# Performance work log

Hardware: AMD Instinct MI355X
Metric: run time of the kernel (lower is better)

## Reference

```python
import jax, jax.numpy as jnp
import numpy as np

B, H, W = 8, 512, 512          # batch, detector grid
M_PER_B = 32768
N = B * M_PER_B
C_IN, C_OUT, RED = 64, 128, 4
EPS = 1e-5


def setup_inputs() -> dict:
    key = jax.random.key(0)
    ks = jax.random.split(key, 8)
    # unique active-site indices per batch (permutation of flat grid cells)
    rng = np.random.default_rng(0)
    rows = []
    for b in range(B):
        flat = rng.permutation(H * W)[:M_PER_B]
        y, x = flat // W, flat % W
        rows.append(np.stack([np.full(M_PER_B, b), y, x], axis=1))
    indices = jnp.asarray(np.concatenate(rows, 0), dtype=jnp.int32)  # [N,3]

    feats = jax.random.normal(ks[0], (N, C_IN), jnp.float32)
    s1 = 1.0 / np.sqrt(9 * C_IN)
    s2 = 1.0 / np.sqrt(9 * C_OUT)
    return {
        "feats": feats,
        "indices": indices,
        "bn1_g": jnp.ones((C_IN,), jnp.float32),
        "bn1_b": jnp.zeros((C_IN,), jnp.float32),
        "w1": jax.random.normal(ks[1], (9, C_IN, C_OUT), jnp.float32) * s1,
        "bn2_g": jnp.ones((C_OUT,), jnp.float32),
        "bn2_b": jnp.zeros((C_OUT,), jnp.float32),
        "w2": jax.random.normal(ks[2], (9, C_OUT, C_OUT), jnp.float32) * s2,
        "fc1_w": jax.random.normal(ks[3], (C_OUT // RED, C_OUT), jnp.float32) / np.sqrt(C_OUT),
        "fc1_b": jnp.zeros((C_OUT // RED,), jnp.float32),
        "fc2_w": jax.random.normal(ks[4], (C_OUT, C_OUT // RED), jnp.float32) / np.sqrt(C_OUT // RED),
        "fc2_b": jnp.zeros((C_OUT,), jnp.float32),
        "w_skip": jax.random.normal(ks[5], (C_IN, C_OUT), jnp.float32) / np.sqrt(C_IN),
    }


def build_rulebook(indices):
    """Neighbor point-ids for each 3x3 offset. Returns ids [N,9], mask [N,9]."""
    n = indices.shape[0]
    b, y, x = indices[:, 0], indices[:, 1], indices[:, 2]
    grid = jnp.full((B, H, W), -1, jnp.int32).at[b, y, x].set(
        jnp.arange(n, dtype=jnp.int32))
    ids, masks = [], []
    for dy in (-1, 0, 1):
        for dx in (-1, 0, 1):
            ny, nx = y + dy, x + dx
            inb = (ny >= 0) & (ny < H) & (nx >= 0) & (nx < W)
            nid = grid[b, jnp.clip(ny, 0, H - 1), jnp.clip(nx, 0, W - 1)]
            m = inb & (nid >= 0)
            ids.append(jnp.where(m, nid, 0))
            masks.append(m)
    return jnp.stack(ids, 1), jnp.stack(masks, 1)


def subm_conv(f, nbr_ids, nbr_mask, w):
    """Submanifold 3x3 conv: gather-GEMM-scatter over active sites."""
    out = jnp.zeros((f.shape[0], w.shape[2]), f.dtype)
    for k in range(w.shape[0]):  # fixed 9 kernel offsets
        g = jnp.where(nbr_mask[:, k:k + 1], f[nbr_ids[:, k]], 0.0)
        out = out + g @ w[k]
    return out


def batchnorm(x, g, b):
    m = jnp.mean(x, 0)
    v = jnp.var(x, 0)  # biased, matches torch BN training normalization
    return (x - m) * jax.lax.rsqrt(v + EPS) * g + b


def reference(feats, indices, bn1_g, bn1_b, w1, bn2_g, bn2_b, w2,
              fc1_w, fc1_b, fc2_w, fc2_b, w_skip):
    nbr_ids, nbr_mask = build_rulebook(indices)  # shared indice_key rulebook
    bidx = indices[:, 0]

    out = jax.nn.relu(batchnorm(feats, bn1_g, bn1_b))
    out = subm_conv(out, nbr_ids, nbr_mask, w1)
    out = jax.nn.relu(batchnorm(out, bn2_g, bn2_b))
    out = subm_conv(out, nbr_ids, nbr_mask, w2)

    # SE: scatter-mean pool per event, FC-ReLU-FC-Sigmoid, per-site rescale
    pooled = jax.ops.segment_sum(out, bidx, num_segments=B)
    counts = jax.ops.segment_sum(jnp.ones((out.shape[0], 1), out.dtype), bidx,
                                 num_segments=B)
    pooled = pooled / jnp.clip(counts, 1.0, None)
    se = jax.nn.sigmoid(jax.nn.relu(pooled @ fc1_w.T + fc1_b) @ fc2_w.T + fc2_b)
    out = out * se[bidx]

    identity = feats @ w_skip  # 1x1 subm conv skip (in_ch != out_ch)
    return out + identity
```

## Files before the change

### kernel.cpp

```cpp
#include <hip/hip_runtime.h>
#include <math.h>

#define NPTS 262144
#define BB 8
#define HH 512
#define WW 512
#define EPSV 1e-5f

typedef short short8v __attribute__((ext_vector_type(8)));
typedef short short4v __attribute__((ext_vector_type(4)));
typedef float float4v __attribute__((ext_vector_type(4)));
typedef unsigned short ushort;
typedef ushort ushort8v __attribute__((ext_vector_type(8)));

static __device__ __forceinline__ ushort f2bf(float f) {
  union { float f; unsigned u; } v;
  v.f = f;
  unsigned r = v.u + 0x7fffu + ((v.u >> 16) & 1u);
  return (ushort)(r >> 16);
}

static __device__ __forceinline__ float bf2f(ushort h) {
  union { unsigned u; float f; } v;
  v.u = ((unsigned)h) << 16;
  return v.f;
}


__global__ __launch_bounds__(256) void k_scatter(const int* __restrict__ idx,
                                                 int* __restrict__ grid) {
  int i = blockIdx.x * 256 + threadIdx.x;
  int b = idx[i * 3 + 0], y = idx[i * 3 + 1], x = idx[i * 3 + 2];
  grid[(b * HH + y) * WW + x] = i;
}

__global__ __launch_bounds__(256) void k_rulebook(const int* __restrict__ idx,
                                                  const int* __restrict__ grid,
                                                  int* __restrict__ nbrT) {
  int i = blockIdx.x * 256 + threadIdx.x;
  int b = idx[i * 3 + 0], y = idx[i * 3 + 1], x = idx[i * 3 + 2];
  int t = 0;
  #pragma unroll
  for (int dy = -1; dy <= 1; ++dy) {
    #pragma unroll
    for (int dx = -1; dx <= 1; ++dx) {
      int ny = y + dy, nx = x + dx;
      int v = -1;
      if (ny >= 0 && ny < HH && nx >= 0 && nx < WW)
        v = grid[(b * HH + ny) * WW + nx];
      nbrT[(size_t)t * NPTS + i] = v;
      ++t;
    }
  }
}


__global__ __launch_bounds__(256) void k_stats64(const float* __restrict__ x,
                                                 float* __restrict__ sum,
                                                 float* __restrict__ ssum) {
  __shared__ float red_s[4][64];
  __shared__ float red_q[4][64];
  const int tid = threadIdx.x;
  const int lane = tid & 63;
  const int wave = tid >> 6;
  const int c4 = lane & 15;
  const int rq = lane >> 4;
  long long base = (long long)blockIdx.x * 256;
  float s0 = 0.f, s1 = 0.f, s2 = 0.f, s3 = 0.f;
  float q0 = 0.f, q1 = 0.f, q2 = 0.f, q3 = 0.f;
  for (int r = wave * 4 + rq; r < 256; r += 16) {
    float4 v = *(const float4*)(x + (base + r) * 64 + c4 * 4);
    s0 += v.x; s1 += v.y; s2 += v.z; s3 += v.w;
    q0 += v.x * v.x; q1 += v.y * v.y; q2 += v.z * v.z; q3 += v.w * v.w;
  }
  s0 += __shfl_xor(s0, 16, 64); s0 += __shfl_xor(s0, 32, 64);
  s1 += __shfl_xor(s1, 16, 64); s1 += __shfl_xor(s1, 32, 64);
  s2 += __shfl_xor(s2, 16, 64); s2 += __shfl_xor(s2, 32, 64);
  s3 += __shfl_xor(s3, 16, 64); s3 += __shfl_xor(s3, 32, 64);
  q0 += __shfl_xor(q0, 16, 64); q0 += __shfl_xor(q0, 32, 64);
  q1 += __shfl_xor(q1, 16, 64); q1 += __shfl_xor(q1, 32, 64);
  q2 += __shfl_xor(q2, 16, 64); q2 += __shfl_xor(q2, 32, 64);
  q3 += __shfl_xor(q3, 16, 64); q3 += __shfl_xor(q3, 32, 64);
  if (rq == 0) {
    red_s[wave][c4 * 4 + 0] = s0; red_s[wave][c4 * 4 + 1] = s1;
    red_s[wave][c4 * 4 + 2] = s2; red_s[wave][c4 * 4 + 3] = s3;
    red_q[wave][c4 * 4 + 0] = q0; red_q[wave][c4 * 4 + 1] = q1;
    red_q[wave][c4 * 4 + 2] = q2; red_q[wave][c4 * 4 + 3] = q3;
  }
  __syncthreads();
  if (tid < 64) {
    float ts = red_s[0][tid] + red_s[1][tid] + red_s[2][tid] + red_s[3][tid];
    float tq = red_q[0][tid] + red_q[1][tid] + red_q[2][tid] + red_q[3][tid];
    atomicAdd(&sum[tid], ts);
    atomicAdd(&ssum[tid], tq);
  }
}

template <int CI>
__global__ void k_finalize(const float* __restrict__ sum, const float* __restrict__ ssum,
                           const float* __restrict__ gam, const float* __restrict__ bet,
                           float* __restrict__ sc, float* __restrict__ sh) {
  int c = threadIdx.x;
  if (c < CI) {
    float m = sum[c] * (1.f / NPTS);
    float v = ssum[c] * (1.f / NPTS) - m * m;
    float s = gam[c] * rsqrtf(v + EPSV);
    sc[c] = s;
    sh[c] = bet[c] - m * s;
  }
}


__global__ __launch_bounds__(256) void k_norm1(const float* __restrict__ x,
                                               const float* __restrict__ sc,
                                               const float* __restrict__ sh,
                                               ushort* __restrict__ y) {
  long long i = ((long long)blockIdx.x * 256 + threadIdx.x) * 8;
  int c = (int)(i & 63);
  float4 a = *(const float4*)(x + i);
  float4 b = *(const float4*)(x + i + 4);
  float4 s0 = *(const float4*)(sc + c);
  float4 s1 = *(const float4*)(sc + c + 4);
  float4 h0 = *(const float4*)(sh + c);
  float4 h1 = *(const float4*)(sh + c + 4);
  ushort8v o;
  o[0] = f2bf(fmaxf(a.x * s0.x + h0.x, 0.f));
  o[1] = f2bf(fmaxf(a.y * s0.y + h0.y, 0.f));
  o[2] = f2bf(fmaxf(a.z * s0.z + h0.z, 0.f));
  o[3] = f2bf(fmaxf(a.w * s0.w + h0.w, 0.f));
  o[4] = f2bf(fmaxf(b.x * s1.x + h1.x, 0.f));
  o[5] = f2bf(fmaxf(b.y * s1.y + h1.y, 0.f));
  o[6] = f2bf(fmaxf(b.z * s1.z + h1.z, 0.f));
  o[7] = f2bf(fmaxf(b.w * s1.w + h1.w, 0.f));
  *(ushort8v*)(y + i) = o;
}

__global__ __launch_bounds__(256) void k_norm2(ushort* __restrict__ x,
                                               const float* __restrict__ sc,
                                               const float* __restrict__ sh) {
  long long i = ((long long)blockIdx.x * 256 + threadIdx.x) * 8;
  int c = (int)(i & 127);
  ushort8v v = *(const ushort8v*)(x + i);
  float4 s0 = *(const float4*)(sc + c);
  float4 s1 = *(const float4*)(sc + c + 4);
  float4 h0 = *(const float4*)(sh + c);
  float4 h1 = *(const float4*)(sh + c + 4);
  ushort8v o;
  o[0] = f2bf(fmaxf(bf2f(v[0]) * s0.x + h0.x, 0.f));
  o[1] = f2bf(fmaxf(bf2f(v[1]) * s0.y + h0.y, 0.f));
  o[2] = f2bf(fmaxf(bf2f(v[2]) * s0.z + h0.z, 0.f));
  o[3] = f2bf(fmaxf(bf2f(v[3]) * s0.w + h0.w, 0.f));
  o[4] = f2bf(fmaxf(bf2f(v[4]) * s1.x + h1.x, 0.f));
  o[5] = f2bf(fmaxf(bf2f(v[5]) * s1.y + h1.y, 0.f));
  o[6] = f2bf(fmaxf(bf2f(v[6]) * s1.z + h1.z, 0.f));
  o[7] = f2bf(fmaxf(bf2f(v[7]) * s1.w + h1.w, 0.f));
  *(ushort8v*)(x + i) = o;
}


__global__ __launch_bounds__(256) void k_wprep(const float* __restrict__ w,
                                               ushort* __restrict__ wt,
                                               int taps, int ci) {
  int i = blockIdx.x * 256 + threadIdx.x;
  int total = taps * ci * 128;
  if (i < total) {
    int t = i / (ci * 128);
    int rem = i - t * ci * 128;
    int c = rem >> 7;
    int o = rem & 127;
    wt[((size_t)t * 128 + o) * ci + c] = f2bf(w[i]);
  }
}


template <int CI, typename DstT, int EPI>
__global__ __launch_bounds__(256) void k_convp(const ushort* __restrict__ src,
                                               const int* __restrict__ nbrT,
                                               const ushort* __restrict__ wt,
                                               DstT* __restrict__ dst,
                                               float* __restrict__ e0,
                                               float* __restrict__ e1) {
  constexpr int CHUNKS = CI / 8;
  constexpr int RPI    = 64 / CHUNKS;
  constexpr int NSTG   = 32 / RPI;
  __shared__ ushort As[128 * CI];

  const int tid = threadIdx.x;
  int bidx = blockIdx.x;
  bidx = (bidx & 7) * ((NPTS / 128) / 8) + (bidx >> 3);
  const int base = bidx * 128;
  const int lane = tid & 63;
  const int wave = tid >> 6;
  const int wm = wave & 1, wn = wave >> 1;
  const int m_base = wm * 64, n_base = wn * 64;
  const int fm = lane & 15;
  const int fq = lane >> 4;

  const int s_rl = lane / CHUNKS;
  const int s_c  = lane % CHUNKS;
  const int srow0 = wave * 32 + s_rl;

  float4v acc[4][4];
  #pragma unroll
  for (int i = 0; i < 4; ++i)
    #pragma unroll
    for (int j = 0; j < 4; ++j) acc[i][j] = (float4v){0.f, 0.f, 0.f, 0.f};

  int nr[2][NSTG];
  uint4 g[NSTG];

  #pragma unroll
  for (int i = 0; i < NSTG; ++i)
    nr[0][i] = nbrT[base + srow0 + i * RPI];
  #pragma unroll
  for (int i = 0; i < NSTG; ++i)
    nr[1][i] = nbrT[(size_t)NPTS + base + srow0 + i * RPI];

  #pragma unroll
  for (int i = 0; i < NSTG; ++i) {
    int nid = nr[0][i];
    uint4 gv = {0u, 0u, 0u, 0u};
    if (nid >= 0) gv = *(const uint4*)(src + (size_t)nid * CI + s_c * 8);
    g[i] = gv;
  }
  #pragma unroll
  for (int i = 0; i < NSTG; ++i) {
    int row = srow0 + i * RPI;
    *(uint4*)(&As[row * CI + ((s_c ^ (row & 7)) << 3)]) = g[i];
  }
  __syncthreads();

  #pragma unroll
  for (int k = 0; k < 9; ++k) {
    if (k < 8) {
      #pragma unroll
      for (int i = 0; i < NSTG; ++i) {
        int nid = nr[(k + 1) & 1][i];
        uint4 gv = {0u, 0u, 0u, 0u};
        if (nid >= 0) gv = *(const uint4*)(src + (size_t)nid * CI + s_c * 8);
        g[i] = gv;
      }
    }
    if (k < 7) {
      #pragma unroll
      for (int i = 0; i < NSTG; ++i)
        nr[k & 1][i] = nbrT[(size_t)(k + 2) * NPTS + base + srow0 + i * RPI];
    }

    const ushort* wrow = wt + ((size_t)k * 128 + n_base + fm) * CI + fq * 8;
    #pragma unroll
    for (int kc = 0; kc < CI / 32; ++kc) {
      short8v af[4], bfr[4];
      #pragma unroll
      for (int mi = 0; mi < 4; ++mi) {
        int R = m_base + mi * 16 + fm;
        af[mi] = *(const short8v*)(&As[R * CI + (((kc * 4 + fq) ^ (fm & 7)) << 3)]);
      }
      #pragma unroll
      for (int ni = 0; ni < 4; ++ni)
        bfr[ni] = *(const short8v*)(wrow + ni * 16 * CI + kc * 32);
      #pragma unroll
      for (int mi = 0; mi < 4; ++mi)
        #pragma unroll
        for (int ni = 0; ni < 4; ++ni)
          acc[mi][ni] = __builtin_amdgcn_mfma_f32_16x16x32_bf16(af[mi], bfr[ni], acc[mi][ni], 0, 0, 0);
    }

    if (k < 8) {
      __syncthreads();
      #pragma unroll
      for (int i = 0; i < NSTG; ++i) {
        int row = srow0 + i * RPI;
        *(uint4*)(&As[row * CI + ((s_c ^ (row & 7)) << 3)]) = g[i];
      }
      __syncthreads();
    }
  }

  float es[4], ess[4];
  if constexpr (EPI) {
    #pragma unroll
    for (int ni = 0; ni < 4; ++ni) { es[ni] = 0.f; ess[ni] = 0.f; }
  }
  #pragma unroll
  for (int mi = 0; mi < 4; ++mi) {
    #pragma unroll
    for (int ni = 0; ni < 4; ++ni) {
      int pt = base + m_base + mi * 16 + fq * 4;
      int co = n_base + ni * 16 + fm;
      float4v c = acc[mi][ni];
      #pragma unroll
      for (int r = 0; r < 4; ++r) {
        if constexpr (sizeof(DstT) == 4) {
          ((float*)dst)[(size_t)(pt + r) * 128 + co] = c[r];
          if constexpr (EPI == 2) es[ni] += c[r];
        } else {
          ushort h = f2bf(c[r]);
          ((ushort*)dst)[(size_t)(pt + r) * 128 + co] = h;
          if constexpr (EPI == 1) {
            float v = bf2f(h);
            es[ni] += v;
            ess[ni] += v * v;
          }
        }
      }
    }
  }

  if constexpr (EPI) {
    #pragma unroll
    for (int ni = 0; ni < 4; ++ni) {
      float s = es[ni];
      s += __shfl_xor(s, 16, 64);
      s += __shfl_xor(s, 32, 64);
      float q = 0.f;
      if constexpr (EPI == 1) {
        q = ess[ni];
        q += __shfl_xor(q, 16, 64);
        q += __shfl_xor(q, 32, 64);
      }
      if (fq == 0) {
        int co = n_base + ni * 16 + fm;
        if constexpr (EPI == 1) {
          atomicAdd(&e0[co], s);
          atomicAdd(&e1[co], q);
        } else {
          int b = base >> 15;
          atomicAdd(&e0[b * 128 + co], s);
        }
      }
    }
  }
}


template <typename SrcT, typename DstT, int CI, int TAPS, bool ACT, int EPI>
__global__ __launch_bounds__(256) void k_conv(const SrcT* __restrict__ src,
                                              const float* __restrict__ scale,
                                              const float* __restrict__ shift,
                                              const int* __restrict__ nbrT,
                                              const ushort* __restrict__ wt,
                                              DstT* __restrict__ dst,
                                              float* __restrict__ e0,
                                              float* __restrict__ e1) {
  constexpr int SA = CI + 8;
  __shared__ ushort As[128 * SA];
  __shared__ ushort Bs[128 * SA];
  __shared__ float s_sc[CI], s_sh[CI];

  const int tid = threadIdx.x;
  const int base = blockIdx.x * 128;
  const int lane = tid & 63;
  const int wave = tid >> 6;
  const int wm = wave & 1, wn = wave >> 1;
  const int m_base = wm * 64, n_base = wn * 64;
  const int fm = lane & 15;
  const int fq = lane >> 4;

  if constexpr (ACT) {
    for (int c = tid; c < CI; c += 256) {
      s_sc[c] = scale[c];
      s_sh[c] = shift[c];
    }
  }
  __syncthreads();

  float4v acc[4][4];
  #pragma unroll
  for (int i = 0; i < 4; ++i)
    #pragma unroll
    for (int j = 0; j < 4; ++j) acc[i][j] = (float4v){0.f, 0.f, 0.f, 0.f};

  const int srow_i = tid >> 1;
  const int shalf = tid & 1;
  const int c0 = shalf * (CI / 2);

  for (int k = 0; k < TAPS; ++k) {
    if (k) __syncthreads();

    int nid;
    if constexpr (TAPS == 1) {
      nid = base + srow_i;
    } else {
      nid = nbrT[(size_t)k * NPTS + base + srow_i];
    }
    ushort* arow = &As[srow_i * SA + c0];
    if (nid >= 0) {
      const SrcT* gsrc = src + (size_t)nid * CI + c0;
      if constexpr (sizeof(SrcT) == 4) {
        #pragma unroll
        for (int j = 0; j < CI / 2; j += 4) {
          float4 v = *(const float4*)((const float*)gsrc + j);
          if constexpr (ACT) {
            int c = c0 + j;
            v.x = fmaxf(v.x * s_sc[c + 0] + s_sh[c + 0], 0.f);
            v.y = fmaxf(v.y * s_sc[c + 1] + s_sh[c + 1], 0.f);
            v.z = fmaxf(v.z * s_sc[c + 2] + s_sh[c + 2], 0.f);
            v.w = fmaxf(v.w * s_sc[c + 3] + s_sh[c + 3], 0.f);
          }
          short4v o = {(short)f2bf(v.x), (short)f2bf(v.y), (short)f2bf(v.z), (short)f2bf(v.w)};
          *(short4v*)(arow + j) = o;
        }
      } else {
        #pragma unroll
        for (int j = 0; j < CI / 2; j += 8) {
          ushort8v raw = *(const ushort8v*)((const ushort*)gsrc + j);
          short8v o;
          #pragma unroll
          for (int e = 0; e < 8; ++e) {
            float f = bf2f(raw[e]);
            if constexpr (ACT) {
              int c = c0 + j + e;
              f = fmaxf(f * s_sc[c] + s_sh[c], 0.f);
            }
            o[e] = (short)f2bf(f);
          }
          *(short8v*)(arow + j) = o;
        }
      }
    } else {
      #pragma unroll
      for (int j = 0; j < CI / 2; j += 4)
        *(short4v*)(arow + j) = (short4v){0, 0, 0, 0};
    }

    {
      const ushort* wrow = wt + ((size_t)k * 128 + srow_i) * CI + c0;
      ushort* brow = &Bs[srow_i * SA + c0];
      #pragma unroll
      for (int j = 0; j < CI / 2; j += 8)
        *(uint4*)(brow + j) = *(const uint4*)(wrow + j);
    }
    __syncthreads();

    #pragma unroll
    for (int kc = 0; kc < CI / 32; ++kc) {
      short8v af[4], bf[4];
      #pragma unroll
      for (int mi = 0; mi < 4; ++mi)
        af[mi] = *(const short8v*)(&As[(m_base + mi * 16 + fm) * SA + kc * 32 + fq * 8]);
      #pragma unroll
      for (int ni = 0; ni < 4; ++ni)
        bf[ni] = *(const short8v*)(&Bs[(n_base + ni * 16 + fm) * SA + kc * 32 + fq * 8]);
      #pragma unroll
      for (int mi = 0; mi < 4; ++mi)
        #pragma unroll
        for (int ni = 0; ni < 4; ++ni)
          acc[mi][ni] = __builtin_amdgcn_mfma_f32_16x16x32_bf16(af[mi], bf[ni], acc[mi][ni], 0, 0, 0);
    }
  }

  float es[4], ess[4];
  if constexpr (EPI) {
    #pragma unroll
    for (int ni = 0; ni < 4; ++ni) { es[ni] = 0.f; ess[ni] = 0.f; }
  }
  #pragma unroll
  for (int mi = 0; mi < 4; ++mi) {
    #pragma unroll
    for (int ni = 0; ni < 4; ++ni) {
      int pt = base + m_base + mi * 16 + fq * 4;
      int co = n_base + ni * 16 + fm;
      float4v c = acc[mi][ni];
      #pragma unroll
      for (int r = 0; r < 4; ++r) {
        if constexpr (sizeof(DstT) == 4) {
          ((float*)dst)[(size_t)(pt + r) * 128 + co] = c[r];
          if constexpr (EPI == 2) es[ni] += c[r];
        } else {
          ushort h = f2bf(c[r]);
          ((ushort*)dst)[(size_t)(pt + r) * 128 + co] = h;
          if constexpr (EPI == 1) {
            float v = bf2f(h);
            es[ni] += v;
            ess[ni] += v * v;
          }
        }
      }
    }
  }

  if constexpr (EPI) {
    #pragma unroll
    for (int ni = 0; ni < 4; ++ni) {
      float s = es[ni];
      s += __shfl_xor(s, 16, 64);
      s += __shfl_xor(s, 32, 64);
      float q = 0.f;
      if constexpr (EPI == 1) {
        q = ess[ni];
        q += __shfl_xor(q, 16, 64);
        q += __shfl_xor(q, 32, 64);
      }
      if (fq == 0) {
        int co = n_base + ni * 16 + fm;
        if constexpr (EPI == 1) {
          atomicAdd(&e0[co], s);
          atomicAdd(&e1[co], q);
        } else {
          int b = base >> 15;
          atomicAdd(&e0[b * 128 + co], s);
        }
      }
    }
  }
}


__global__ __launch_bounds__(256) void k_se(const float* __restrict__ pooled,
                                            const float* __restrict__ fc1w,
                                            const float* __restrict__ fc1b,
                                            const float* __restrict__ fc2w,
                                            const float* __restrict__ fc2b,
                                            float* __restrict__ se) {
  __shared__ float h[8][32];
  int tid = threadIdx.x;
  int b = tid >> 5, j = tid & 31;
  float s = fc1b[j];
  for (int c = 0; c < 128; ++c)
    s += pooled[b * 128 + c] * (1.f / 32768.f) * fc1w[j * 128 + c];
  h[b][j] = fmaxf(s, 0.f);
  __syncthreads();
  for (int t = tid; t < 1024; t += 256) {
    int bb = t >> 7, c = t & 127;
    float s2 = fc2b[c];
    #pragma unroll
    for (int jj = 0; jj < 32; ++jj) s2 += h[bb][jj] * fc2w[c * 32 + jj];
    se[t] = 1.f / (1.f + expf(-s2));
  }
}

__global__ __launch_bounds__(256) void k_final(float* __restrict__ out,
                                               const ushort* __restrict__ id,
                                               const float* __restrict__ se) {
  long long i = ((long long)blockIdx.x * 256 + threadIdx.x) * 4;
  int co = (int)(i & 127);
  long long rowi = i >> 7;
  int b = (int)(rowi >> 15);
  float4 o = *(const float4*)(out + i);
  ushort dh[4];
  *(uint2*)dh = *(const uint2*)(id + i);
  float4 s = *(const float4*)(se + b * 128 + co);
  o.x = o.x * s.x + bf2f(dh[0]);
  o.y = o.y * s.y + bf2f(dh[1]);
  o.z = o.z * s.z + bf2f(dh[2]);
  o.w = o.w * s.w + bf2f(dh[3]);
  *(float4*)(out + i) = o;
}


extern "C" void kernel_launch(void* const* d_in, const int* in_sizes, int n_in,
                              void* d_out, int out_size, void* d_ws, size_t ws_size,
                              hipStream_t stream) {
  const float* feats = (const float*)d_in[0];
  const int* indices = (const int*)d_in[1];
  const float* bn1_g = (const float*)d_in[2];
  const float* bn1_b = (const float*)d_in[3];
  const float* w1    = (const float*)d_in[4];
  const float* bn2_g = (const float*)d_in[5];
  const float* bn2_b = (const float*)d_in[6];
  const float* w2    = (const float*)d_in[7];
  const float* fc1w  = (const float*)d_in[8];
  const float* fc1b  = (const float*)d_in[9];
  const float* fc2w  = (const float*)d_in[10];
  const float* fc2b  = (const float*)d_in[11];
  const float* wskip = (const float*)d_in[12];
  float* out = (float*)d_out;

  char* p = (char*)d_ws;
  int* nbrT = (int*)p;      p += (size_t)NPTS * 9 * 4;
  float* stats = (float*)p; p += 4096 * 4;
  ushort* wt1 = (ushort*)p; p += (size_t)9 * 128 * 64 * 2;
  ushort* wt2 = (ushort*)p; p += (size_t)9 * 128 * 128 * 2;
  ushort* wts = (ushort*)p; p += (size_t)128 * 64 * 2;
  p = (char*)(((size_t)p + 255) & ~(size_t)255);

  float* sum1 = stats, *ss1 = stats + 64, *sc1 = stats + 128, *sh1 = stats + 192;
  float* sum2 = stats + 256, *ss2 = stats + 384, *sc2 = stats + 512, *sh2 = stats + 640;
  float* pooled = stats + 768;
  float* se = stats + 1792;

  size_t fixed = (size_t)(p - (char*)d_ws);
  size_t need_new = fixed + (size_t)NPTS * 64 * 2 + (size_t)NPTS * 128 * 2;
  bool big = ws_size >= need_new;

  hipMemsetAsync(stats, 0, 4096 * 4, stream);

  if (big) {
    int* grid_i = (int*)p;
    ushort* featsn = (ushort*)p;
    ushort* out1 = (ushort*)(p + (size_t)NPTS * 64 * 2);

    hipMemsetAsync(grid_i, 0xFF, (size_t)BB * HH * WW * 4, stream);
    k_scatter<<<NPTS / 256, 256, 0, stream>>>(indices, grid_i);
    k_rulebook<<<NPTS / 256, 256, 0, stream>>>(indices, grid_i, nbrT);

    k_wprep<<<(9 * 64 * 128 + 255) / 256, 256, 0, stream>>>(w1, wt1, 9, 64);
    k_wprep<<<(9 * 128 * 128 + 255) / 256, 256, 0, stream>>>(w2, wt2, 9, 128);
    k_wprep<<<(64 * 128 + 255) / 256, 256, 0, stream>>>(wskip, wts, 1, 64);

    k_stats64<<<NPTS / 256, 256, 0, stream>>>(feats, sum1, ss1);
    k_finalize<64><<<1, 64, 0, stream>>>(sum1, ss1, bn1_g, bn1_b, sc1, sh1);

    k_norm1<<<NPTS * 64 / 8 / 256, 256, 0, stream>>>(feats, sc1, sh1, featsn);

    k_convp<64, ushort, 1><<<NPTS / 128, 256, 0, stream>>>(
        featsn, nbrT, wt1, out1, sum2, ss2);

    k_finalize<128><<<1, 128, 0, stream>>>(sum2, ss2, bn2_g, bn2_b, sc2, sh2);

    k_norm2<<<NPTS * 128 / 8 / 256, 256, 0, stream>>>(out1, sc2, sh2);

    k_convp<128, float, 2><<<NPTS / 128, 256, 0, stream>>>(
        out1, nbrT, wt2, out, pooled, nullptr);

    k_conv<float, ushort, 64, 1, false, 0><<<NPTS / 128, 256, 0, stream>>>(
        feats, nullptr, nullptr, nullptr, wts, out1, nullptr, nullptr);

    k_se<<<1, 256, 0, stream>>>(pooled, fc1w, fc1b, fc2w, fc2b, se);
    k_final<<<NPTS * 128 / 1024, 256, 0, stream>>>(out, out1, se);
  } else {
    int* grid_i = (int*)p;
    ushort* out1 = (ushort*)p;

    hipMemsetAsync(grid_i, 0xFF, (size_t)BB * HH * WW * 4, stream);
    k_scatter<<<NPTS / 256, 256, 0, stream>>>(indices, grid_i);
    k_rulebook<<<NPTS / 256, 256, 0, stream>>>(indices, grid_i, nbrT);

    k_wprep<<<(9 * 64 * 128 + 255) / 256, 256, 0, stream>>>(w1, wt1, 9, 64);
    k_wprep<<<(9 * 128 * 128 + 255) / 256, 256, 0, stream>>>(w2, wt2, 9, 128);
    k_wprep<<<(64 * 128 + 255) / 256, 256, 0, stream>>>(wskip, wts, 1, 64);

    k_stats64<<<NPTS / 256, 256, 0, stream>>>(feats, sum1, ss1);
    k_finalize<64><<<1, 64, 0, stream>>>(sum1, ss1, bn1_g, bn1_b, sc1, sh1);

    k_conv<float, ushort, 64, 9, true, 1><<<NPTS / 128, 256, 0, stream>>>(
        feats, sc1, sh1, nbrT, wt1, out1, sum2, ss2);

    k_finalize<128><<<1, 128, 0, stream>>>(sum2, ss2, bn2_g, bn2_b, sc2, sh2);

    k_conv<ushort, float, 128, 9, true, 2><<<NPTS / 128, 256, 0, stream>>>(
        out1, sc2, sh2, nbrT, wt2, out, pooled, nullptr);

    k_conv<float, ushort, 64, 1, false, 0><<<NPTS / 128, 256, 0, stream>>>(
        feats, nullptr, nullptr, nullptr, wts, out1, nullptr, nullptr);

    k_se<<<1, 256, 0, stream>>>(pooled, fc1w, fc1b, fc2w, fc2b, se);
    k_final<<<NPTS * 128 / 1024, 256, 0, stream>>>(out, out1, se);
  }
}
```

Measured before the change: 689.1 us.

## Stage per-tap weight tiles in LDS and make neighbor gathers branchless

The gather conv kernel now loads each tap's 128xCI weight slice into a second swizzled LDS buffer, prefetched alongside the neighbor features. MFMA B operands then come from LDS instead of per-wave global reads. Gathers for missing neighbors now read row 0 unconditionally and are zeroed at LDS store time, which removes divergent branches. The cost is double the LDS footprint (64KB for CI=128), which may cut occupancy, plus some wasted loads for empty neighbors.

```diff
diff --git a/kernel.cpp b/kernel.cpp
--- a/kernel.cpp
+++ b/kernel.cpp
@@ -174,16 +174,17 @@
 
 
 template <int CI, typename DstT, int EPI>
-__global__ __launch_bounds__(256) void k_convp(const ushort* __restrict__ src,
-                                               const int* __restrict__ nbrT,
-                                               const ushort* __restrict__ wt,
-                                               DstT* __restrict__ dst,
-                                               float* __restrict__ e0,
-                                               float* __restrict__ e1) {
+__global__ __launch_bounds__(256) void k_convp2(const ushort* __restrict__ src,
+                                                const int* __restrict__ nbrT,
+                                                const ushort* __restrict__ wt,
+                                                DstT* __restrict__ dst,
+                                                float* __restrict__ e0,
+                                                float* __restrict__ e1) {
   constexpr int CHUNKS = CI / 8;
   constexpr int RPI    = 64 / CHUNKS;
   constexpr int NSTG   = 32 / RPI;
   __shared__ ushort As[128 * CI];
+  __shared__ ushort Bs[128 * CI];
 
   const int tid = threadIdx.x;
   int bidx = blockIdx.x;
@@ -207,7 +208,8 @@
     for (int j = 0; j < 4; ++j) acc[i][j] = (float4v){0.f, 0.f, 0.f, 0.f};
 
   int nr[2][NSTG];
-  uint4 g[NSTG];
+  uint4 ga[NSTG], gb[NSTG];
+  const uint4 zz = {0u, 0u, 0u, 0u};
 
   #pragma unroll
   for (int i = 0; i < NSTG; ++i)
@@ -219,14 +221,18 @@
   #pragma unroll
   for (int i = 0; i < NSTG; ++i) {
     int nid = nr[0][i];
-    uint4 gv = {0u, 0u, 0u, 0u};
-    if (nid >= 0) gv = *(const uint4*)(src + (size_t)nid * CI + s_c * 8);
-    g[i] = gv;
-  }
+    int cn = nid < 0 ? 0 : nid;
+    ga[i] = *(const uint4*)(src + (size_t)cn * CI + s_c * 8);
+  }
+  #pragma unroll
+  for (int i = 0; i < NSTG; ++i)
+    gb[i] = *(const uint4*)(wt + ((size_t)0 * 128 + srow0 + i * RPI) * CI + s_c * 8);
   #pragma unroll
   for (int i = 0; i < NSTG; ++i) {
     int row = srow0 + i * RPI;
-    *(uint4*)(&As[row * CI + ((s_c ^ (row & 7)) << 3)]) = g[i];
+    int off = row * CI + ((s_c ^ (row & 7)) << 3);
+    *(uint4*)(&As[off]) = (nr[0][i] >= 0) ? ga[i] : zz;
+    *(uint4*)(&Bs[off]) = gb[i];
   }
   __syncthreads();
 
@@ -236,10 +242,12 @@
       #pragma unroll
       for (int i = 0; i < NSTG; ++i) {
         int nid = nr[(k + 1) & 1][i];
-        uint4 gv = {0u, 0u, 0u, 0u};
-        if (nid >= 0) gv = *(const uint4*)(src + (size_t)nid * CI + s_c * 8);
-        g[i] = gv;
-      }
+        int cn = nid < 0 ? 0 : nid;
+        ga[i] = *(const uint4*)(src + (size_t)cn * CI + s_c * 8);
+      }
+      #pragma unroll
+      for (int i = 0; i < NSTG; ++i)
+        gb[i] = *(const uint4*)(wt + ((size_t)(k + 1) * 128 + srow0 + i * RPI) * CI + s_c * 8);
     }
     if (k < 7) {
       #pragma unroll
@@ -247,23 +255,24 @@
         nr[k & 1][i] = nbrT[(size_t)(k + 2) * NPTS + base + srow0 + i * RPI];
     }
 
-    const ushort* wrow = wt + ((size_t)k * 128 + n_base + fm) * CI + fq * 8;
     #pragma unroll
     for (int kc = 0; kc < CI / 32; ++kc) {
-      short8v af[4], bfr[4];
+      short8v af[4], bf[4];
       #pragma unroll
       for (int mi = 0; mi < 4; ++mi) {
         int R = m_base + mi * 16 + fm;
         af[mi] = *(const short8v*)(&As[R * CI + (((kc * 4 + fq) ^ (fm & 7)) << 3)]);
       }
       #pragma unroll
-      for (int ni = 0; ni < 4; ++ni)
-        bfr[ni] = *(const short8v*)(wrow + ni * 16 * CI + kc * 32);
+      for (int ni = 0; ni < 4; ++ni) {
+        int R = n_base + ni * 16 + fm;
+        bf[ni] = *(const short8v*)(&Bs[R * CI + (((kc * 4 + fq) ^ (fm & 7)) << 3)]);
+      }
       #pragma unroll
       for (int mi = 0; mi < 4; ++mi)
         #pragma unroll
         for (int ni = 0; ni < 4; ++ni)
-          acc[mi][ni] = __builtin_amdgcn_mfma_f32_16x16x32_bf16(af[mi], bfr[ni], acc[mi][ni], 0, 0, 0);
+          acc[mi][ni] = __builtin_amdgcn_mfma_f32_16x16x32_bf16(af[mi], bf[ni], acc[mi][ni], 0, 0, 0);
     }
 
     if (k < 8) {
@@ -271,7 +280,9 @@
       #pragma unroll
       for (int i = 0; i < NSTG; ++i) {
         int row = srow0 + i * RPI;
-        *(uint4*)(&As[row * CI + ((s_c ^ (row & 7)) << 3)]) = g[i];
+        int off = row * CI + ((s_c ^ (row & 7)) << 3);
+        *(uint4*)(&As[off]) = (nr[(k + 1) & 1][i] >= 0) ? ga[i] : zz;
+        *(uint4*)(&Bs[off]) = gb[i];
       }
       __syncthreads();
     }
@@ -604,14 +615,14 @@
 
     k_norm1<<<NPTS * 64 / 8 / 256, 256, 0, stream>>>(feats, sc1, sh1, featsn);
 
-    k_convp<64, ushort, 1><<<NPTS / 128, 256, 0, stream>>>(
+    k_convp2<64, ushort, 1><<<NPTS / 128, 256, 0, stream>>>(
         featsn, nbrT, wt1, out1, sum2, ss2);
 
     k_finalize<128><<<1, 128, 0, stream>>>(sum2, ss2, bn2_g, bn2_b, sc2, sh2);
 
     k_norm2<<<NPTS * 128 / 8 / 256, 256, 0, stream>>>(out1, sc2, sh2);
 
-    k_convp<128, float, 2><<<NPTS / 128, 256, 0, stream>>>(
+    k_convp2<128, float, 2><<<NPTS / 128, 256, 0, stream>>>(
         out1, nbrT, wt2, out, pooled, nullptr);
 
     k_conv<float, ushort, 64, 1, false, 0><<<NPTS / 128, 256, 0, stream>>>(
```

Measured after the change: 945.6 us. 37.2% more time.
